# Optimization experiments

Measured on AMD Instinct MI355X. Metric: run time of the kernel, lower is better.

The kernel has to match this reference:

```python
import jax, jax.numpy as jnp
import numpy as np

N = 20000      # num nodes
E = 320000     # num edges (before self loops)
D = 512        # d_model
H = 4          # gnn_heads
C = 256        # gnn_hidden_dim (per-head out channels)
L = 4          # gnn_num_layers
B = 16         # number of graphs in batch
NEG_SLOPE = 0.2
LN_EPS = 1e-5


def setup_inputs() -> dict:
    key = jax.random.key(0)
    ks = jax.random.split(key, 10)
    s = 0.05
    return {
        "x": jax.random.normal(ks[0], (N, D), jnp.float32),
        "edge_index": jax.random.randint(ks[1], (2, E), 0, N, dtype=jnp.int32),
        "batch": jnp.sort(jax.random.randint(ks[2], (N,), 0, B, dtype=jnp.int32)),
        "W0": jax.random.normal(ks[3], (D, H * C), jnp.float32) * s,
        "W_rest": jax.random.normal(ks[4], (L - 1, H * C, H * C), jnp.float32) * s,
        "att_src": jax.random.normal(ks[5], (L, H, C), jnp.float32) * s,
        "att_dst": jax.random.normal(ks[6], (L, H, C), jnp.float32) * s,
        "conv_bias": jnp.zeros((L, H * C), jnp.float32),
        "proj_W": jax.random.normal(ks[7], (H * C, D), jnp.float32) * s,
        "proj_b": jnp.zeros((D,), jnp.float32),
        "ln_gamma": jnp.ones((D,), jnp.float32),
        "ln_beta": jnp.zeros((D,), jnp.float32),
    }


def _gat_layer(x, src, dst, W, a_src, a_dst, b):
    # x: [N, F_in] -> h: [N, H, C]
    h = (x @ W).reshape(N, H, C)
    alpha_src = jnp.einsum('nhc,hc->nh', h, a_src)   # [N, H]
    alpha_dst = jnp.einsum('nhc,hc->nh', h, a_dst)   # [N, H]
    e = jax.nn.leaky_relu(alpha_src[src] + alpha_dst[dst], NEG_SLOPE)  # [Etot, H]
    # per-destination softmax (every node has a self loop, so segments nonempty)
    m = jax.ops.segment_max(e, dst, num_segments=N)
    ex = jnp.exp(e - m[dst])
    denom = jax.ops.segment_sum(ex, dst, num_segments=N)
    alpha = ex / (denom[dst] + 1e-16)                # [Etot, H]
    out = jax.ops.segment_sum(alpha[:, :, None] * h[src], dst, num_segments=N)  # [N, H, C]
    return out.reshape(N, H * C) + b


def reference(x, edge_index, batch, W0, W_rest, att_src, att_dst, conv_bias,
              proj_W, proj_b, ln_gamma, ln_beta):
    # add self loops (PyG GATConv default)
    loop = jnp.arange(N, dtype=edge_index.dtype)
    src = jnp.concatenate([edge_index[0], loop])
    dst = jnp.concatenate([edge_index[1], loop])

    h = x
    for l in range(L):
        W = W0 if l == 0 else W_rest[l - 1]
        h = _gat_layer(h, src, dst, W, att_src[l], att_dst[l], conv_bias[l])
        h = jax.nn.relu(h)  # dropout: eval mode -> identity

    # global mean pool over nodes per graph
    sums = jax.ops.segment_sum(h, batch, num_segments=B)           # [B, H*C]
    counts = jax.ops.segment_sum(jnp.ones((N,), h.dtype), batch, num_segments=B)
    pooled = sums / jnp.maximum(counts, 1.0)[:, None]

    out = pooled @ proj_W + proj_b                                 # [B, D]
    mu = out.mean(-1, keepdims=True)
    var = ((out - mu) ** 2).mean(-1, keepdims=True)
    return (out - mu) / jnp.sqrt(var + LN_EPS) * ln_gamma + ln_beta
```

## Files before the change

kernel.cpp:

```cpp
#include <hip/hip_runtime.h>
#include <hip/hip_bf16.h>
#include <hip/hip_fp8.h>
#include <math.h>

#define Nn 20000
#define Ee 320000
#define Dd 512
#define Hh 4
#define Cc 256
#define Ll 4
#define Bb 16
#define HC 1024
#define ETOT (Ee + Nn)
#define NEG_SLOPE 0.2f
#define LN_EPS 1e-5f
#define NBLK ((Nn + 255) / 256)

typedef __attribute__((ext_vector_type(8))) __bf16 bf16x8;
typedef __attribute__((ext_vector_type(4))) __bf16 bf16x4;
typedef __attribute__((ext_vector_type(4))) float f32x4;
typedef __attribute__((ext_vector_type(2))) float f32x2;

__device__ __forceinline__ f32x4 fp8x4_to_f32(unsigned int v) {
#if __has_builtin(__builtin_amdgcn_cvt_pk_f32_fp8)
    f32x2 lo = __builtin_amdgcn_cvt_pk_f32_fp8((int)v, false);
    f32x2 hi = __builtin_amdgcn_cvt_pk_f32_fp8((int)v, true);
    f32x4 r; r[0] = lo[0]; r[1] = lo[1]; r[2] = hi[0]; r[3] = hi[1];
    return r;
#else
    f32x4 r;
    #pragma unroll
    for (int i = 0; i < 4; ++i) {
        __hip_fp8_e4m3 q; q.__x = (v >> (8 * i)) & 0xff;
        r[i] = (float)q;
    }
    return r;
#endif
}

__device__ __forceinline__ unsigned char f32_to_fp8(float f) {
    return __hip_fp8_e4m3(f).__x;
}


__device__ __forceinline__ void decode_edge(const int* ei, int e, int& s, int& d) {
    if (e < Ee) { s = ei[e]; d = ei[Ee + e]; }
    else        { s = e - Ee; d = e - Ee; }
}

__global__ void count_deg_kernel(const int* __restrict__ ei, int* __restrict__ deg) {
    int e = blockIdx.x * blockDim.x + threadIdx.x;
    if (e >= ETOT) return;
    int s, d; decode_edge(ei, e, s, d);
    atomicAdd(&deg[d], 1);
}

__global__ void scan1_kernel(const int* __restrict__ deg, int* __restrict__ tmp,
                             int* __restrict__ bsum) {
    __shared__ int sd[256];
    int tid = threadIdx.x;
    int i = blockIdx.x * 256 + tid;
    sd[tid] = (i < Nn) ? deg[i] : 0;
    __syncthreads();
    for (int off = 1; off < 256; off <<= 1) {
        int t = (tid >= off) ? sd[tid - off] : 0;
        __syncthreads();
        sd[tid] += t;
        __syncthreads();
    }
    if (i < Nn) tmp[i] = sd[tid];
    if (tid == 255) bsum[blockIdx.x] = sd[255];
}

__global__ void scan2_kernel(int* __restrict__ bsum) {
    __shared__ int sd[256];
    int tid = threadIdx.x;
    sd[tid] = (tid < NBLK) ? bsum[tid] : 0;
    __syncthreads();
    for (int off = 1; off < 256; off <<= 1) {
        int t = (tid >= off) ? sd[tid - off] : 0;
        __syncthreads();
        sd[tid] += t;
        __syncthreads();
    }
    if (tid < NBLK) bsum[tid] = sd[tid];
}

__global__ void scan3_kernel(const int* __restrict__ tmp, const int* __restrict__ bsum,
                             const int* __restrict__ deg,
                             int* __restrict__ row_ptr, int* __restrict__ cursor) {
    int i = blockIdx.x * 256 + threadIdx.x;
    if (i >= Nn) return;
    int boff = (blockIdx.x == 0) ? 0 : bsum[blockIdx.x - 1];
    int incl = tmp[i] + boff;
    row_ptr[i + 1] = incl;
    cursor[i] = incl - deg[i];
    if (i == 0) row_ptr[0] = 0;
}

__global__ void scatter_kernel(const int* __restrict__ ei, int* __restrict__ cursor,
                               int* __restrict__ csr_src) {
    int e = blockIdx.x * blockDim.x + threadIdx.x;
    if (e >= ETOT) return;
    int s, d; decode_edge(ei, e, s, d);
    int pos = atomicAdd(&cursor[d], 1);
    csr_src[pos] = s;
}


__global__ void cast_kernel(const float* __restrict__ in, __bf16* __restrict__ out, int n4) {
    int i = blockIdx.x * blockDim.x + threadIdx.x;
    if (i >= n4) return;
    f32x4 v = ((const f32x4*)in)[i];
    bf16x4 o;
    #pragma unroll
    for (int k = 0; k < 4; ++k) o[k] = (__bf16)v[k];
    ((bf16x4*)out)[i] = o;
}

__global__ void transpose_cast_kernel(const float* __restrict__ W, __bf16* __restrict__ WT,
                                      int K, int N) {
    __shared__ float tile[32][33];
    W  += (size_t)blockIdx.z * K * N;
    WT += (size_t)blockIdx.z * K * N;
    int n0 = blockIdx.x * 32, k0 = blockIdx.y * 32;
    for (int i = threadIdx.y; i < 32; i += 8)
        tile[i][threadIdx.x] = W[(size_t)(k0 + i) * N + n0 + threadIdx.x];
    __syncthreads();
    for (int i = threadIdx.y; i < 32; i += 8)
        WT[(size_t)(n0 + i) * K + k0 + threadIdx.x] = (__bf16)tile[threadIdx.x][i];
}


__device__ __forceinline__ void async16(const __bf16* g, __bf16* l) {
    __builtin_amdgcn_global_load_lds((const __attribute__((address_space(1))) void*)g,
                                     (__attribute__((address_space(3))) void*)l,
                                     16, 0, 0);
}

__global__ __launch_bounds__(256) void mfma_gemm_kernel(
    const __bf16* __restrict__ A,
    const __bf16* __restrict__ BT,
    unsigned char* __restrict__ C8,
    const float* __restrict__ att_s,
    const float* __restrict__ att_d,
    float* __restrict__ aprt_s,
    float* __restrict__ aprt_d,
    int M, int K)
{
    int lin = blockIdx.y * 8 + blockIdx.x;
    int rblk = (lin >> 6) * 8 + (lin & 7);
    int cblk = (lin >> 3) & 7;
    int rowBase = rblk * 128, colBase = cblk * 128;
    if (rowBase >= M) return;

    __shared__ __bf16 As[2][128 * 32];
    __shared__ __bf16 Bs[2][128 * 32];
    int tid = threadIdx.x;
    int wave = tid >> 6, lane = tid & 63;
    int m16 = lane & 15, quad = lane >> 4;
    int waveRow = (wave >> 1) * 64, waveCol = (wave & 1) * 64;

    f32x4 acc[4][4] = {};

    int srow = wave * 32 + (lane >> 2);
    int gch0 = (lane & 3) ^ ((srow >> 1) & 3);
    int gch1 = (lane & 3) ^ (((srow + 16) >> 1) & 3);
    int gr0 = rowBase + srow;       if (gr0 >= M) gr0 = M - 1;
    int gr1 = rowBase + srow + 16;  if (gr1 >= M) gr1 = M - 1;
    int ldsOff = srow * 32 + (lane & 3) * 8;

    for (int k0 = 0; k0 < K; k0 += 64) {
        #pragma unroll
        for (int p = 0; p < 2; ++p) {
            int kp = k0 + p * 32;
            async16(A + (size_t)gr0 * K + kp + gch0 * 8, &As[p][ldsOff]);
            async16(A + (size_t)gr1 * K + kp + gch1 * 8, &As[p][ldsOff + 16 * 32]);
            async16(BT + (size_t)(colBase + srow) * K + kp + gch0 * 8, &Bs[p][ldsOff]);
            async16(BT + (size_t)(colBase + srow + 16) * K + kp + gch1 * 8, &Bs[p][ldsOff + 16 * 32]);
        }
        __syncthreads();
        #pragma unroll
        for (int p = 0; p < 2; ++p) {
            bf16x8 af[4], bfr[4];
            #pragma unroll
            for (int i = 0; i < 4; ++i) {
                int row = waveRow + i * 16 + m16;
                af[i] = *(const bf16x8*)&As[p][row * 32 + (quad ^ ((row >> 1) & 3)) * 8];
                int col = waveCol + i * 16 + m16;
                bfr[i] = *(const bf16x8*)&Bs[p][col * 32 + (quad ^ ((col >> 1) & 3)) * 8];
            }
            #pragma unroll
            for (int i = 0; i < 4; ++i)
                #pragma unroll
                for (int j = 0; j < 4; ++j)
                    acc[i][j] = __builtin_amdgcn_mfma_f32_16x16x32_bf16(af[i], bfr[j], acc[i][j], 0, 0, 0);
        }
        __syncthreads();
    }

    int cbase = colBase + waveCol;
    int head = cbase >> 8;
    int part = (cblk & 1) * 2 + (wave & 1);
    float as4[4], ad4[4];
    #pragma unroll
    for (int j = 0; j < 4; ++j) {
        int off = (cbase + j * 16 + m16) & 255;
        as4[j] = att_s[head * 256 + off];
        ad4[j] = att_d[head * 256 + off];
    }

    #pragma unroll
    for (int i = 0; i < 4; ++i) {
        int r0 = rowBase + waveRow + i * 16 + quad * 4;
        #pragma unroll
        for (int r = 0; r < 4; ++r) {
            int row = r0 + r;
            float ps = 0.f, pd = 0.f;
            #pragma unroll
            for (int j = 0; j < 4; ++j) {
                float h = acc[i][j][r];
                ps += h * as4[j];
                pd += h * ad4[j];
                if (row < M)
                    C8[(size_t)row * HC + colBase + waveCol + j * 16 + m16] = f32_to_fp8(h);
            }
            #pragma unroll
            for (int off = 1; off < 16; off <<= 1) {
                ps += __shfl_xor(ps, off);
                pd += __shfl_xor(pd, off);
            }
            if (m16 == 0 && row < M) {
                aprt_s[((size_t)part * M + row) * 4 + head] = ps;
                aprt_d[((size_t)part * M + row) * 4 + head] = pd;
            }
        }
    }
}


__global__ void alpha_sum_kernel(const float* __restrict__ aprt_s,
                                 const float* __restrict__ aprt_d,
                                 float* __restrict__ asrc, float* __restrict__ adst) {
    int n = blockIdx.x * 256 + threadIdx.x;
    if (n >= Nn) return;
    f32x4 s = {0.f, 0.f, 0.f, 0.f}, d = {0.f, 0.f, 0.f, 0.f};
    #pragma unroll
    for (int p = 0; p < 4; ++p) {
        f32x4 vs = ((const f32x4*)aprt_s)[(size_t)p * Nn + n];
        f32x4 vd = ((const f32x4*)aprt_d)[(size_t)p * Nn + n];
        #pragma unroll
        for (int k = 0; k < 4; ++k) { s[k] += vs[k]; d[k] += vd[k]; }
    }
    ((f32x4*)asrc)[n] = s;
    ((f32x4*)adst)[n] = d;
}


__global__ __launch_bounds__(256) void ew_kernel(const float* __restrict__ asrc,
                                                 const float* __restrict__ adst,
                                                 const int* __restrict__ row_ptr,
                                                 const int* __restrict__ csr_src,
                                                 int2* __restrict__ ceT,
                                                 float* __restrict__ dinv) {
    int grp = threadIdx.x >> 4, lane16 = threadIdx.x & 15;
    int n = blockIdx.x * 16 + grp;
    if (n >= Nn) return;
    int start = row_ptr[n], end = row_ptr[n + 1];
    f32x4 ad = ((const f32x4*)adst)[n];
    f32x4 d = {0.f, 0.f, 0.f, 0.f};
    for (int e = start + lane16; e < end; e += 16) {
        int s = csr_src[e];
        f32x4 as = ((const f32x4*)asrc)[s];
        #pragma unroll
        for (int k = 0; k < 4; ++k) {
            float z = as[k] + ad[k];
            z = (z > 0.f) ? z : NEG_SLOPE * z;
            float ex = __expf(z);
            int2 ce; ce.x = s; ce.y = __float_as_int(ex);
            ceT[(size_t)k * ETOT + e] = ce;
            d[k] += ex;
        }
    }
    #pragma unroll
    for (int off = 8; off > 0; off >>= 1) {
        #pragma unroll
        for (int k = 0; k < 4; ++k) d[k] += __shfl_xor(d[k], off);
    }
    if (lane16 == 0) {
        f32x4 iv;
        #pragma unroll
        for (int k = 0; k < 4; ++k) iv[k] = 1.f / (d[k] + 1e-16f);
        ((f32x4*)dinv)[n] = iv;
    }
}


__global__ __launch_bounds__(256) void agg_slice_kernel(
    const unsigned char* __restrict__ h8,
    const int2* __restrict__ ceT,
    const float* __restrict__ dinv,
    const int* __restrict__ row_ptr,
    const float* __restrict__ bias_l,
    __bf16* __restrict__ outb)
{
    int slice = blockIdx.x;
    int head = slice >> 1;
    int tid = threadIdx.x;
    int nslot = tid >> 3;
    int ch = tid & 7;
    int n = blockIdx.y * 32 + nslot;

    __shared__ int2 ce_sh[1024];
    __shared__ int  rp_sh[33];

    if (tid < 33) rp_sh[tid] = row_ptr[blockIdx.y * 32 + tid];
    __syncthreads();
    int blk_lo = rp_sh[0], blk_hi = rp_sh[32];
    int start = rp_sh[nslot], end = rp_sh[nslot + 1];

    const unsigned char* hs = h8 + slice * 128 + ch * 16;
    const int2* ceh = ceT + (size_t)head * ETOT;
    float acc[16] = {};

    for (int c0 = blk_lo; c0 < blk_hi; c0 += 1024) {
        int c1 = min(c0 + 1024, blk_hi);
        int cnt = c1 - c0;
        for (int i = tid; i < cnt; i += 256)
            ce_sh[i] = ceh[c0 + i];
        __syncthreads();
        int lo = max(start, c0), hi = min(end, c1);
        for (int e = lo; e < hi; ++e) {
            int2 v = ce_sh[e - c0];
            float w = __int_as_float(v.y);
            uint4 u = *(const uint4*)(hs + (size_t)v.x * HC);
            f32x4 a0 = fp8x4_to_f32(u.x), a1 = fp8x4_to_f32(u.y);
            f32x4 a2 = fp8x4_to_f32(u.z), a3 = fp8x4_to_f32(u.w);
            #pragma unroll
            for (int k = 0; k < 4; ++k) {
                acc[k]      += w * a0[k];
                acc[k + 4]  += w * a1[k];
                acc[k + 8]  += w * a2[k];
                acc[k + 12] += w * a3[k];
            }
        }
        __syncthreads();
    }

    float inv = dinv[n * 4 + head];
    bf16x8 o0, o1;
    #pragma unroll
    for (int k = 0; k < 8; ++k) {
        o0[k] = (__bf16)fmaxf(acc[k] * inv + bias_l[slice * 128 + ch * 16 + k], 0.f);
        o1[k] = (__bf16)fmaxf(acc[k + 8] * inv + bias_l[slice * 128 + ch * 16 + 8 + k], 0.f);
    }
    *(bf16x8*)(outb + (size_t)n * HC + slice * 128 + ch * 16) = o0;
    *(bf16x8*)(outb + (size_t)n * HC + slice * 128 + ch * 16 + 8) = o1;
}


__device__ __forceinline__ int lower_bound_batch(const int* __restrict__ batch, int val) {
    int lo = 0, hi = Nn;
    while (lo < hi) { int mid = (lo + hi) >> 1; if (batch[mid] < val) lo = mid + 1; else hi = mid; }
    return lo;
}

__global__ void pool_kernel(const __bf16* __restrict__ h2b, const int* __restrict__ batch,
                            float* __restrict__ pooledP) {
    int b = blockIdx.x, part = blockIdx.y;
    int tid = threadIdx.x;
    int start = lower_bound_batch(batch, b);
    int end   = lower_bound_batch(batch, b + 1);
    int len = end - start;
    int chunk = (len + 7) / 8;
    int s0 = start + part * chunk;
    int s1 = min(s0 + chunk, end);
    float acc[4] = {0.f, 0.f, 0.f, 0.f};
    for (int n = s0; n < s1; ++n) {
        bf16x4 v = ((const bf16x4*)(h2b + (size_t)n * HC))[tid];
        #pragma unroll
        for (int k = 0; k < 4; ++k) acc[k] += (float)v[k];
    }
    #pragma unroll
    for (int k = 0; k < 4; ++k)
        pooledP[((size_t)part * Bb + b) * HC + tid * 4 + k] = acc[k];
}


__global__ __launch_bounds__(512) void proj_partial_kernel(const float* __restrict__ pooledP,
                                                           const int* __restrict__ batch,
                                                           const float* __restrict__ projW,
                                                           float* __restrict__ projP) {
    int b = blockIdx.x, part = blockIdx.y;
    int d = threadIdx.x;
    __shared__ float psum[HC];
    int start = lower_bound_batch(batch, b);
    int end   = lower_bound_batch(batch, b + 1);
    float inv = 1.0f / fmaxf((float)(end - start), 1.0f);
    for (int k = d; k < HC; k += 512) {
        float s = 0.f;
        #pragma unroll
        for (int p = 0; p < 8; ++p) s += pooledP[((size_t)p * Bb + b) * HC + k];
        psum[k] = s * inv;
    }
    __syncthreads();
    float acc = 0.f;
    int k0 = part * 128;
    for (int k = k0; k < k0 + 128; ++k)
        acc += psum[k] * projW[(size_t)k * Dd + d];
    projP[((size_t)part * Bb + b) * Dd + d] = acc;
}

__global__ __launch_bounds__(512) void ln_kernel(const float* __restrict__ projP,
                                                 const float* __restrict__ projb,
                                                 const float* __restrict__ gamma,
                                                 const float* __restrict__ beta,
                                                 float* __restrict__ out) {
    int b = blockIdx.x;
    int d = threadIdx.x;
    __shared__ float red[512];
    float o = projb[d];
    #pragma unroll
    for (int p = 0; p < 8; ++p) o += projP[((size_t)p * Bb + b) * Dd + d];
    red[d] = o;
    __syncthreads();
    for (int off = 256; off > 0; off >>= 1) {
        if (d < off) red[d] += red[d + off];
        __syncthreads();
    }
    float mu = red[0] / (float)Dd;
    __syncthreads();
    float df = o - mu;
    red[d] = df * df;
    __syncthreads();
    for (int off = 256; off > 0; off >>= 1) {
        if (d < off) red[d] += red[d + off];
        __syncthreads();
    }
    float var = red[0] / (float)Dd;
    out[b * Dd + d] = df / sqrtf(var + LN_EPS) * gamma[d] + beta[d];
}


extern "C" void kernel_launch(void* const* d_in, const int* in_sizes, int n_in,
                              void* d_out, int out_size, void* d_ws, size_t ws_size,
                              hipStream_t stream) {
    const float* x         = (const float*)d_in[0];
    const int*   ei        = (const int*)d_in[1];
    const int*   batch     = (const int*)d_in[2];
    const float* W0        = (const float*)d_in[3];
    const float* W_rest    = (const float*)d_in[4];
    const float* att_src   = (const float*)d_in[5];
    const float* att_dst   = (const float*)d_in[6];
    const float* conv_bias = (const float*)d_in[7];
    const float* proj_W    = (const float*)d_in[8];
    const float* proj_b    = (const float*)d_in[9];
    const float* ln_gamma  = (const float*)d_in[10];
    const float* ln_beta   = (const float*)d_in[11];
    float* out = (float*)d_out;

    char* ws = (char*)d_ws;
    size_t off = 0;
    auto alloc = [&](size_t bytes) {
        void* p = ws + off;
        off = (off + bytes + 255) & ~(size_t)255;
        return p;
    };
    unsigned char* h8 = (unsigned char*)alloc((size_t)Nn * HC);
    __bf16* h2b     = (__bf16*)alloc((size_t)Nn * HC * 2);
    __bf16* xb      = (__bf16*)alloc((size_t)Nn * Dd * 2);
    __bf16* W0T     = (__bf16*)alloc((size_t)HC * Dd * 2);
    __bf16* WrT     = (__bf16*)alloc((size_t)3 * HC * HC * 2);
    float*  aprt_s  = (float*)alloc((size_t)4 * Nn * Hh * 4);
    float*  aprt_d  = (float*)alloc((size_t)4 * Nn * Hh * 4);
    float*  asrc    = (float*)alloc((size_t)Nn * Hh * 4);
    float*  adst    = (float*)alloc((size_t)Nn * Hh * 4);
    int2*   ceT     = (int2*)alloc((size_t)Hh * ETOT * 8);
    float*  dinv    = (float*)alloc((size_t)Nn * Hh * 4);
    int*    deg     = (int*)alloc((size_t)Nn * 4);
    int*    tmp     = (int*)alloc((size_t)Nn * 4);
    int*    bsum    = (int*)alloc((size_t)256 * 4);
    int*    row_ptr = (int*)alloc((size_t)(Nn + 1) * 4);
    int*    cursor  = (int*)alloc((size_t)Nn * 4);
    int*    csr_src = (int*)alloc((size_t)ETOT * 4);
    float*  pooledP = (float*)alloc((size_t)8 * Bb * HC * 4);
    float*  projP   = (float*)alloc((size_t)8 * Bb * Dd * 4);
    (void)ws_size; (void)in_sizes; (void)n_in; (void)out_size;

    hipMemsetAsync(deg, 0, (size_t)Nn * 4, stream);
    count_deg_kernel<<<(ETOT + 255) / 256, 256, 0, stream>>>(ei, deg);
    scan1_kernel<<<NBLK, 256, 0, stream>>>(deg, tmp, bsum);
    scan2_kernel<<<1, 256, 0, stream>>>(bsum);
    scan3_kernel<<<NBLK, 256, 0, stream>>>(tmp, bsum, deg, row_ptr, cursor);
    scatter_kernel<<<(ETOT + 255) / 256, 256, 0, stream>>>(ei, cursor, csr_src);

    cast_kernel<<<(Nn * Dd / 4 + 255) / 256, 256, 0, stream>>>(x, xb, Nn * Dd / 4);
    transpose_cast_kernel<<<dim3(HC / 32, Dd / 32, 1), dim3(32, 8), 0, stream>>>(W0, W0T, Dd, HC);
    transpose_cast_kernel<<<dim3(HC / 32, HC / 32, 3), dim3(32, 8), 0, stream>>>(W_rest, WrT, HC, HC);

    dim3 gemm_grid(8, 160);
    for (int l = 0; l < Ll; ++l) {
        const __bf16* Afeat = (l == 0) ? xb : h2b;
        int K = (l == 0) ? Dd : HC;
        const __bf16* BT = (l == 0) ? W0T : (WrT + (size_t)(l - 1) * HC * HC);
        mfma_gemm_kernel<<<gemm_grid, 256, 0, stream>>>(
            Afeat, BT, h8, att_src + l * HC, att_dst + l * HC, aprt_s, aprt_d, Nn, K);
        alpha_sum_kernel<<<NBLK, 256, 0, stream>>>(aprt_s, aprt_d, asrc, adst);
        ew_kernel<<<(Nn + 15) / 16, 256, 0, stream>>>(asrc, adst, row_ptr, csr_src, ceT, dinv);
        agg_slice_kernel<<<dim3(8, Nn / 32), 256, 0, stream>>>(
            h8, ceT, dinv, row_ptr, conv_bias + l * HC, h2b);
    }

    pool_kernel<<<dim3(Bb, 8), 256, 0, stream>>>(h2b, batch, pooledP);
    proj_partial_kernel<<<dim3(Bb, 8), 512, 0, stream>>>(pooledP, batch, proj_W, projP);
    ln_kernel<<<Bb, 512, 0, stream>>>(projP, proj_b, ln_gamma, ln_beta, out);
}
```

Measured before the change: 633.4 us.

## Fuse edge-weight computation into aggregation kernel, drop ceT/dinv buffers

Removes the separate edge-weight kernel that wrote per-head (src, exp) pairs and inverse denominators to global memory. The aggregation kernel now computes each edge's leaky-relu exp weight while staging edges into shared memory, using a binary search over the block's row pointers to find the destination node. It also accumulates the softmax denominator per node locally. This saves one launch and the global write/read of the edge-weight array per layer, but the exp is recomputed in each of the two slices per head, and the softmax max-subtraction is still omitted as before.

```diff
diff --git a/kernel.cpp b/kernel.cpp
--- a/kernel.cpp
+++ b/kernel.cpp
@@ -257,50 +257,12 @@
 }
 
 
-__global__ __launch_bounds__(256) void ew_kernel(const float* __restrict__ asrc,
-                                                 const float* __restrict__ adst,
-                                                 const int* __restrict__ row_ptr,
-                                                 const int* __restrict__ csr_src,
-                                                 int2* __restrict__ ceT,
-                                                 float* __restrict__ dinv) {
-    int grp = threadIdx.x >> 4, lane16 = threadIdx.x & 15;
-    int n = blockIdx.x * 16 + grp;
-    if (n >= Nn) return;
-    int start = row_ptr[n], end = row_ptr[n + 1];
-    f32x4 ad = ((const f32x4*)adst)[n];
-    f32x4 d = {0.f, 0.f, 0.f, 0.f};
-    for (int e = start + lane16; e < end; e += 16) {
-        int s = csr_src[e];
-        f32x4 as = ((const f32x4*)asrc)[s];
-        #pragma unroll
-        for (int k = 0; k < 4; ++k) {
-            float z = as[k] + ad[k];
-            z = (z > 0.f) ? z : NEG_SLOPE * z;
-            float ex = __expf(z);
-            int2 ce; ce.x = s; ce.y = __float_as_int(ex);
-            ceT[(size_t)k * ETOT + e] = ce;
-            d[k] += ex;
-        }
-    }
-    #pragma unroll
-    for (int off = 8; off > 0; off >>= 1) {
-        #pragma unroll
-        for (int k = 0; k < 4; ++k) d[k] += __shfl_xor(d[k], off);
-    }
-    if (lane16 == 0) {
-        f32x4 iv;
-        #pragma unroll
-        for (int k = 0; k < 4; ++k) iv[k] = 1.f / (d[k] + 1e-16f);
-        ((f32x4*)dinv)[n] = iv;
-    }
-}
-
-
 __global__ __launch_bounds__(256) void agg_slice_kernel(
     const unsigned char* __restrict__ h8,
-    const int2* __restrict__ ceT,
-    const float* __restrict__ dinv,
+    const float* __restrict__ asrc,
+    const float* __restrict__ adst,
     const int* __restrict__ row_ptr,
+    const int* __restrict__ csr_src,
     const float* __restrict__ bias_l,
     __bf16* __restrict__ outb)
 {
@@ -311,28 +273,40 @@
     int ch = tid & 7;
     int n = blockIdx.y * 32 + nslot;
 
-    __shared__ int2 ce_sh[1024];
-    __shared__ int  rp_sh[33];
-
-    if (tid < 33) rp_sh[tid] = row_ptr[blockIdx.y * 32 + tid];
+    __shared__ int2  ce_sh[1024];
+    __shared__ int   rp_sh[33];
+    __shared__ float ad_sh[32];
+
+    int base = blockIdx.y * 32;
+    if (tid < 33) rp_sh[tid] = row_ptr[base + tid];
+    if (tid < 32) ad_sh[tid] = adst[(base + tid) * 4 + head];
     __syncthreads();
     int blk_lo = rp_sh[0], blk_hi = rp_sh[32];
     int start = rp_sh[nslot], end = rp_sh[nslot + 1];
 
     const unsigned char* hs = h8 + slice * 128 + ch * 16;
-    const int2* ceh = ceT + (size_t)head * ETOT;
     float acc[16] = {};
+    float dsum = 0.f;
 
     for (int c0 = blk_lo; c0 < blk_hi; c0 += 1024) {
         int c1 = min(c0 + 1024, blk_hi);
         int cnt = c1 - c0;
-        for (int i = tid; i < cnt; i += 256)
-            ce_sh[i] = ceh[c0 + i];
+        for (int i = tid; i < cnt; i += 256) {
+            int eg = c0 + i;
+            int s = csr_src[eg];
+            int lo = 0, hi2 = 32;
+            while (hi2 - lo > 1) { int mid = (lo + hi2) >> 1; if (rp_sh[mid] <= eg) lo = mid; else hi2 = mid; }
+            float z = asrc[s * 4 + head] + ad_sh[lo];
+            z = (z > 0.f) ? z : NEG_SLOPE * z;
+            int2 v; v.x = s; v.y = __float_as_int(__expf(z));
+            ce_sh[i] = v;
+        }
         __syncthreads();
         int lo = max(start, c0), hi = min(end, c1);
         for (int e = lo; e < hi; ++e) {
             int2 v = ce_sh[e - c0];
             float w = __int_as_float(v.y);
+            dsum += w;
             uint4 u = *(const uint4*)(hs + (size_t)v.x * HC);
             f32x4 a0 = fp8x4_to_f32(u.x), a1 = fp8x4_to_f32(u.y);
             f32x4 a2 = fp8x4_to_f32(u.z), a3 = fp8x4_to_f32(u.w);
@@ -347,7 +321,7 @@
         __syncthreads();
     }
 
-    float inv = dinv[n * 4 + head];
+    float inv = 1.f / (dsum + 1e-16f);
     bf16x8 o0, o1;
     #pragma unroll
     for (int k = 0; k < 8; ++k) {
@@ -475,8 +449,6 @@
     float*  aprt_d  = (float*)alloc((size_t)4 * Nn * Hh * 4);
     float*  asrc    = (float*)alloc((size_t)Nn * Hh * 4);
     float*  adst    = (float*)alloc((size_t)Nn * Hh * 4);
-    int2*   ceT     = (int2*)alloc((size_t)Hh * ETOT * 8);
-    float*  dinv    = (float*)alloc((size_t)Nn * Hh * 4);
     int*    deg     = (int*)alloc((size_t)Nn * 4);
     int*    tmp     = (int*)alloc((size_t)Nn * 4);
     int*    bsum    = (int*)alloc((size_t)256 * 4);
@@ -506,9 +478,8 @@
         mfma_gemm_kernel<<<gemm_grid, 256, 0, stream>>>(
             Afeat, BT, h8, att_src + l * HC, att_dst + l * HC, aprt_s, aprt_d, Nn, K);
         alpha_sum_kernel<<<NBLK, 256, 0, stream>>>(aprt_s, aprt_d, asrc, adst);
-        ew_kernel<<<(Nn + 15) / 16, 256, 0, stream>>>(asrc, adst, row_ptr, csr_src, ceT, dinv);
         agg_slice_kernel<<<dim3(8, Nn / 32), 256, 0, stream>>>(
-            h8, ceT, dinv, row_ptr, conv_bias + l * HC, h2b);
+            h8, asrc, adst, row_ptr, csr_src, conv_bias + l * HC, h2b);
     }
 
     pool_kernel<<<dim3(Bb, 8), 256, 0, stream>>>(h2b, batch, pooledP);
```

After: 634.6 us. About the same (+0.2%).
